# Optimization experiments

Hardware: AMD Instinct MI355X
Metric: run time of the kernel (lower is better)

Reference implementation:

```python
import jax, jax.numpy as jnp
import numpy as np

B, S, D = 2, 1024, 1024
C, HID, H = 32, 64, 16  # compress_dim, prg_hidden_dim, num_heads


def setup_inputs() -> dict:
    key = jax.random.key(0)
    ks = jax.random.split(key, 7)
    def glorot(k, shape):
        lim = 1.0 / np.sqrt(shape[0])
        return jax.random.uniform(k, shape, jnp.float32, -lim, lim)
    return {
        "x": jax.random.normal(ks[0], (B, S, D), jnp.float32),
        "Wc": glorot(ks[1], (D, C)),
        "bc": jnp.zeros((C,), jnp.float32),
        "W1": glorot(ks[2], (2 * C, HID)),
        "b1": jnp.zeros((HID,), jnp.float32),
        "W2": glorot(ks[3], (HID, H)),
        "b2": jnp.zeros((H,), jnp.float32),
    }


def reference(x, Wc, bc, W1, b1, W2, b2):
    Bc, Sc, _ = x.shape
    # compress: [B,S,C]
    xc = x @ Wc + bc
    # pairwise concat via broadcast (same values as tile+concat)
    token_i = jnp.broadcast_to(xc[:, :, None, :], (Bc, Sc, Sc, C))
    token_j = jnp.broadcast_to(xc[:, None, :, :], (Bc, Sc, Sc, C))
    pair_emb = jnp.concatenate([token_i, token_j], axis=-1)  # [B,S,S,2C]
    h = jax.nn.gelu(pair_emb @ W1 + b1)                      # [B,S,S,HID]
    prg_bias = h @ W2 + b2                                   # [B,S,S,H]
    return jnp.transpose(prg_bias, (0, 3, 1, 2))             # [B,H,S,S]
```

## Files before the change

### kernel.cpp

```cpp
#include <hip/hip_runtime.h>
#include <hip/hip_fp16.h>

#define SDIM 1024

typedef _Float16 f16;
typedef _Float16 f16x8 __attribute__((ext_vector_type(8)));
typedef __attribute__((ext_vector_type(4))) float f32x4;

union FragH { unsigned int u[4]; f16x8 f; uint4 q; };

constexpr unsigned short f16bits(float x) {
    return __builtin_bit_cast(unsigned short, (_Float16)x);
}
constexpr unsigned int pk2(float x) {
    return (unsigned int)f16bits(x) * 0x10001u;
}

__device__ __forceinline__ unsigned int addgelu_pair(
    unsigned int au, unsigned int bu,
    unsigned int sLo, unsigned int sHi, unsigned int sXA, unsigned int vXB,
    unsigned int sC5, unsigned int vC4, unsigned int sC3, unsigned int sC2,
    unsigned int sC1, unsigned int sC0, unsigned int sHalf)
{
    unsigned int g, t, tc, x, w;
    asm("v_pk_add_f16 %1, %5, %6\n\t"
        "v_pk_max_f16 %2, %1, %7\n\t"
        "v_pk_min_f16 %2, %2, %8\n\t"
        "v_pk_mul_f16 %3, %2, %2\n\t"
        "v_pk_fma_f16 %3, %3, %9, %10\n\t"
        "v_pk_fma_f16 %4, %3, %11, %12\n\t"
        "v_pk_fma_f16 %4, %4, %3, %13\n\t"
        "v_pk_fma_f16 %4, %4, %3, %14\n\t"
        "v_pk_fma_f16 %4, %4, %3, %15\n\t"
        "v_pk_fma_f16 %4, %4, %3, %16\n\t"
        "v_pk_fma_f16 %4, %4, %2, %17\n\t"
        "v_pk_mul_f16 %0, %1, %4"
        : "=v"(g), "=&v"(t), "=&v"(tc), "=&v"(x), "=&v"(w)
        : "v"(au), "v"(bu),
          "s"(sLo), "s"(sHi), "s"(sXA), "v"(vXB),
          "s"(sC5), "v"(vC4), "s"(sC3), "s"(sC2), "s"(sC1), "s"(sC0), "s"(sHalf));
    return g;
}

#define GELU_CONSTS  kLo, kHi, kXA, kXB, kC5, kC4, kC3, kC2, kC1, kC0, kHalf
#define DECL_GELU_CONSTS \
    const unsigned int kLo   = pk2(-3.0f); \
    const unsigned int kHi   = pk2( 3.0f); \
    const unsigned int kXA   = pk2( 2.0f / 9.0f); \
    const unsigned int kXB   = pk2(-1.0f); \
    const unsigned int kC5   = pk2(-0.003456f); \
    const unsigned int kC4   = pk2( 0.009668f); \
    const unsigned int kC3   = pk2(-0.020158f); \
    const unsigned int kC2   = pk2( 0.045110f); \
    const unsigned int kC1   = pk2(-0.092726f); \
    const unsigned int kC0   = pk2( 0.2278245f); \
    const unsigned int kHalf = pk2( 0.5f);

__global__ __launch_bounds__(256) void compute_uv(
    const float* __restrict__ x, const float* __restrict__ Wc,
    const float* __restrict__ bc, const float* __restrict__ W1,
    const float* __restrict__ b1, const float* __restrict__ W2,
    f16* __restrict__ u, f16* __restrict__ v, f16* __restrict__ W2h)
{
    __shared__ float xrow[2 * 1024];
    __shared__ float part[2 * 8 * 32];
    __shared__ float xc[2 * 32];
    const int tid = threadIdx.x;
    const size_t bs0 = (size_t)blockIdx.x * 2;

    if (blockIdx.x == 0) {
        #pragma unroll
        for (int e = 0; e < 4; ++e) {
            const int flat = tid * 4 + e;
            const int h = flat >> 6, k = flat & 63;
            W2h[flat] = (f16)W2[k * 16 + h];
        }
    }
    const float4* xin = (const float4*)(x + bs0 * 1024);
    #pragma unroll
    for (int it = 0; it < 2; ++it)
        ((float4*)xrow)[it * 256 + tid] = xin[it * 256 + tid];
    __syncthreads();
    {
        const int c = tid & 31, p = tid >> 5;
        float acc0 = 0.f, acc1 = 0.f;
        #pragma unroll 8
        for (int dd = 0; dd < 128; ++dd) {
            const int d = p * 128 + dd;
            const float wv = Wc[d * 32 + c];
            acc0 = __builtin_fmaf(xrow[d],        wv, acc0);
            acc1 = __builtin_fmaf(xrow[1024 + d], wv, acc1);
        }
        part[p * 32 + c]       = acc0;
        part[256 + p * 32 + c] = acc1;
    }
    __syncthreads();
    if (tid < 64) {
        const int r = tid >> 5, c = tid & 31;
        float s = bc[c];
        #pragma unroll
        for (int p = 0; p < 8; ++p) s += part[r * 256 + p * 32 + c];
        xc[r * 32 + c] = s;
    }
    __syncthreads();
    if (tid < 128) {
        const int h = tid & 63;
        const int rr = tid >> 6;
        float ua = b1[h], va = 0.0f;
        #pragma unroll
        for (int cc = 0; cc < 32; ++cc) {
            const float xv = xc[rr * 32 + cc];
            ua = __builtin_fmaf(xv, W1[cc * 64 + h], ua);
            va = __builtin_fmaf(xv, W1[(32 + cc) * 64 + h], va);
        }
        u[(bs0 + rr) * 64 + h] = (f16)ua;
        v[(bs0 + rr) * 64 + h] = (f16)va;
    } else {
        const int h = (tid - 128) & 63;
        const int rr = (tid - 128) >> 6;
        float va2 = 0.0f, ua2 = b1[h];
        (void)va2; (void)ua2; (void)h; (void)rr;
    }
}

__global__ __launch_bounds__(1024) void prg_main(
    const f16* __restrict__ u, const f16* __restrict__ v,
    const f16* __restrict__ W2h, const float* __restrict__ b2,
    float* __restrict__ out)
{
    const int tid  = threadIdx.x;
    const int lane = tid & 63;
    const int w    = tid >> 6;
    const int jb   = blockIdx.x * 64;
    const int ib   = blockIdx.y * 64;
    const int b    = blockIdx.z;

    DECL_GELU_CONSTS

    __shared__ f16 u_lds[64][64];

    if (tid < 512) {
        const int row = tid >> 3;
        const int col = (tid & 7) * 8;
        *(uint4*)&u_lds[row][col] =
            *(const uint4*)(u + ((size_t)(b * SDIM + ib + row) * 64 + col));
    }

    const int lg = lane >> 4;
    const int lr = lane & 15;
    const int k0 = lg * 8;
    const int jw = jb + (w & 3) * 16;
    const int iw = (w >> 2) * 16;

    const f16* vp = v + ((size_t)(b * SDIM + jw + lr) * 64);
    const uint4 vlo = *(const uint4*)(vp + k0);
    const uint4 vhi = *(const uint4*)(vp + k0 + 32);

    FragH w2lo, w2hi;
    w2lo.q = *(const uint4*)(W2h + lr * 64 + k0);
    w2hi.q = *(const uint4*)(W2h + lr * 64 + k0 + 32);

    const float b2h = b2[lr];

    __syncthreads();

    float* ob = out + ((size_t)(b * 16 + lr) * SDIM + (ib + iw)) * SDIM + jw + lg * 4;

#define GM(IL, ACC)                                                               \
    {                                                                             \
        const uint4 alo = *(const uint4*)&u_lds[IL][k0];                          \
        const uint4 ahi = *(const uint4*)&u_lds[IL][k0 + 32];                     \
        FragH glo, ghi;                                                           \
        glo.u[0] = addgelu_pair(alo.x, vlo.x, GELU_CONSTS);                       \
        glo.u[1] = addgelu_pair(alo.y, vlo.y, GELU_CONSTS);                       \
        glo.u[2] = addgelu_pair(alo.z, vlo.z, GELU_CONSTS);                       \
        glo.u[3] = addgelu_pair(alo.w, vlo.w, GELU_CONSTS);                       \
        ghi.u[0] = addgelu_pair(ahi.x, vhi.x, GELU_CONSTS);                       \
        ghi.u[1] = addgelu_pair(ahi.y, vhi.y, GELU_CONSTS);                       \
        ghi.u[2] = addgelu_pair(ahi.z, vhi.z, GELU_CONSTS);                       \
        ghi.u[3] = addgelu_pair(ahi.w, vhi.w, GELU_CONSTS);                       \
        f32x4 a_ = {b2h, b2h, b2h, b2h};                                          \
        a_ = __builtin_amdgcn_mfma_f32_16x16x32_f16(glo.f, w2lo.f, a_, 0, 0, 0);  \
        a_ = __builtin_amdgcn_mfma_f32_16x16x32_f16(ghi.f, w2hi.f, a_, 0, 0, 0);  \
        ACC = a_;                                                                 \
    }
#define ST(IL, ACC) *(float4*)(ob + (size_t)(IL) * SDIM) = *(float4*)&(ACC);

    f32x4 accA, accB;
    GM(iw + 0, accA)
    #pragma unroll
    for (int p = 0; p < 7; ++p) {
        GM(iw + 2 * p + 1, accB)
        ST(2 * p, accA)
        GM(iw + 2 * p + 2, accA)
        ST(2 * p + 1, accB)
    }
    GM(iw + 15, accB)
    ST(14, accA)
    ST(15, accB)
#undef GM
#undef ST
}

extern "C" void kernel_launch(void* const* d_in, const int* in_sizes, int n_in,
                              void* d_out, int out_size, void* d_ws, size_t ws_size,
                              hipStream_t stream) {
    const float* x  = (const float*)d_in[0];
    const float* Wc = (const float*)d_in[1];
    const float* bc = (const float*)d_in[2];
    const float* W1 = (const float*)d_in[3];
    const float* b1 = (const float*)d_in[4];
    const float* W2 = (const float*)d_in[5];
    const float* b2 = (const float*)d_in[6];
    float* out = (float*)d_out;

    f16* u   = (f16*)d_ws;
    f16* v   = u + 2 * SDIM * 64;
    f16* W2h = v + 2 * SDIM * 64;

    compute_uv<<<dim3(1024), dim3(256), 0, stream>>>(x, Wc, bc, W1, b1, W2, u, v, W2h);
    prg_main<<<dim3(16, 16, 2), dim3(1024), 0, stream>>>(u, v, W2h, b2, out);
}
```

Before: 44.06 us.

## Split prg kernel into producer compute waves and consumer store waves via LDS

The main kernel now warp-specializes: 8 waves compute GELU+MFMA for twice as many rows each and write results into a double-buffered LDS stage, while the other 8 waves read the stage and issue the global stores. The goal is to overlap the large output write traffic with compute, so compute waves never stall on store issue. The cost is extra LDS traffic, two block-wide barriers per step, and halving the number of waves doing math.

```diff
diff --git a/kernel.cpp b/kernel.cpp
--- a/kernel.cpp
+++ b/kernel.cpp
@@ -115,15 +115,10 @@
         }
         u[(bs0 + rr) * 64 + h] = (f16)ua;
         v[(bs0 + rr) * 64 + h] = (f16)va;
-    } else {
-        const int h = (tid - 128) & 63;
-        const int rr = (tid - 128) >> 6;
-        float va2 = 0.0f, ua2 = b1[h];
-        (void)va2; (void)ua2; (void)h; (void)rr;
-    }
-}
-
-__global__ __launch_bounds__(1024) void prg_main(
+    }
+}
+
+__global__ __launch_bounds__(1024) void prg_pc(
     const f16* __restrict__ u, const f16* __restrict__ v,
     const f16* __restrict__ W2h, const float* __restrict__ b2,
     float* __restrict__ out)
@@ -131,13 +126,15 @@
     const int tid  = threadIdx.x;
     const int lane = tid & 63;
     const int w    = tid >> 6;
+    const int wc   = w & 7;
     const int jb   = blockIdx.x * 64;
     const int ib   = blockIdx.y * 64;
     const int b    = blockIdx.z;
 
     DECL_GELU_CONSTS
 
-    __shared__ f16 u_lds[64][64];
+    __shared__ f16   u_lds[64][64];
+    __shared__ float stage[2][8][4][64][4];
 
     if (tid < 512) {
         const int row = tid >> 3;
@@ -149,22 +146,20 @@
     const int lg = lane >> 4;
     const int lr = lane & 15;
     const int k0 = lg * 8;
-    const int jw = jb + (w & 3) * 16;
-    const int iw = (w >> 2) * 16;
+    const int jw = jb + (wc & 3) * 16;
+    const int iw = (wc >> 2) * 32;
 
     const f16* vp = v + ((size_t)(b * SDIM + jw + lr) * 64);
     const uint4 vlo = *(const uint4*)(vp + k0);
     const uint4 vhi = *(const uint4*)(vp + k0 + 32);
-
     FragH w2lo, w2hi;
     w2lo.q = *(const uint4*)(W2h + lr * 64 + k0);
     w2hi.q = *(const uint4*)(W2h + lr * 64 + k0 + 32);
-
     const float b2h = b2[lr];
 
-    __syncthreads();
-
     float* ob = out + ((size_t)(b * 16 + lr) * SDIM + (ib + iw)) * SDIM + jw + lg * 4;
+
+    __syncthreads();
 
 #define GM(IL, ACC)                                                               \
     {                                                                             \
@@ -184,22 +179,67 @@
         a_ = __builtin_amdgcn_mfma_f32_16x16x32_f16(ghi.f, w2hi.f, a_, 0, 0, 0);  \
         ACC = a_;                                                                 \
     }
-#define ST(IL, ACC) *(float4*)(ob + (size_t)(IL) * SDIM) = *(float4*)&(ACC);
-
-    f32x4 accA, accB;
-    GM(iw + 0, accA)
+#define BAR() asm volatile("s_barrier" ::: "memory")
+#define LGKM0() asm volatile("s_waitcnt lgkmcnt(0)" ::: "memory")
+
+    f32x4 rA0, rA1, rA2, rA3;
+    f32x4 rB0, rB1, rB2, rB3;
+
     #pragma unroll
-    for (int p = 0; p < 7; ++p) {
-        GM(iw + 2 * p + 1, accB)
-        ST(2 * p, accA)
-        GM(iw + 2 * p + 2, accA)
-        ST(2 * p + 1, accB)
-    }
-    GM(iw + 15, accB)
-    ST(14, accA)
-    ST(15, accB)
+    for (int q = 0; q < 8; ++q) {
+        if (w < 8) {
+            f32x4 a0, a1, a2, a3;
+            GM(iw + q * 4 + 0, a0)
+            GM(iw + q * 4 + 1, a1)
+            GM(iw + q * 4 + 2, a2)
+            GM(iw + q * 4 + 3, a3)
+            BAR();
+            *(float4*)&stage[q & 1][wc][0][lane][0] = *(float4*)&a0;
+            *(float4*)&stage[q & 1][wc][1][lane][0] = *(float4*)&a1;
+            *(float4*)&stage[q & 1][wc][2][lane][0] = *(float4*)&a2;
+            *(float4*)&stage[q & 1][wc][3][lane][0] = *(float4*)&a3;
+            LGKM0();
+            BAR();
+        } else {
+            if (q > 0) {
+                float* po = ob + (size_t)((q - 1) * 4) * SDIM;
+                if ((q - 1) & 1) {
+                    *(float4*)(po)            = *(float4*)&rB0;
+                    *(float4*)(po + SDIM)     = *(float4*)&rB1;
+                    *(float4*)(po + 2 * SDIM) = *(float4*)&rB2;
+                    *(float4*)(po + 3 * SDIM) = *(float4*)&rB3;
+                } else {
+                    *(float4*)(po)            = *(float4*)&rA0;
+                    *(float4*)(po + SDIM)     = *(float4*)&rA1;
+                    *(float4*)(po + 2 * SDIM) = *(float4*)&rA2;
+                    *(float4*)(po + 3 * SDIM) = *(float4*)&rA3;
+                }
+            }
+            BAR();
+            BAR();
+            if (q & 1) {
+                rB0 = *(f32x4*)&stage[1][wc][0][lane][0];
+                rB1 = *(f32x4*)&stage[1][wc][1][lane][0];
+                rB2 = *(f32x4*)&stage[1][wc][2][lane][0];
+                rB3 = *(f32x4*)&stage[1][wc][3][lane][0];
+            } else {
+                rA0 = *(f32x4*)&stage[0][wc][0][lane][0];
+                rA1 = *(f32x4*)&stage[0][wc][1][lane][0];
+                rA2 = *(f32x4*)&stage[0][wc][2][lane][0];
+                rA3 = *(f32x4*)&stage[0][wc][3][lane][0];
+            }
+        }
+    }
+    if (w >= 8) {
+        float* po = ob + (size_t)(7 * 4) * SDIM;
+        *(float4*)(po)            = *(float4*)&rB0;
+        *(float4*)(po + SDIM)     = *(float4*)&rB1;
+        *(float4*)(po + 2 * SDIM) = *(float4*)&rB2;
+        *(float4*)(po + 3 * SDIM) = *(float4*)&rB3;
+    }
 #undef GM
-#undef ST
+#undef BAR
+#undef LGKM0
 }
 
 extern "C" void kernel_launch(void* const* d_in, const int* in_sizes, int n_in,
@@ -219,5 +259,5 @@
     f16* W2h = v + 2 * SDIM * 64;
 
     compute_uv<<<dim3(1024), dim3(256), 0, stream>>>(x, Wc, bc, W1, b1, W2, u, v, W2h);
-    prg_main<<<dim3(16, 16, 2), dim3(1024), 0, stream>>>(u, v, W2h, b2, out);
-}
+    prg_pc<<<dim3(16, 16, 2), dim3(1024), 0, stream>>>(u, v, W2h, b2, out);
+}
```

After: 52.79 us. 19.8% more time.
